# Performance work log

Hardware: AMD Instinct MI355X
Metric: run time of the kernel (lower is better)

## Reference

```python
import jax, jax.numpy as jnp
import numpy as np

B, D, F = 2048, 512, 16384
K = 3
AUX_THR = 0.7
EPS = 1e-8


def setup_inputs() -> dict:
    key = jax.random.key(0)
    ks = jax.random.split(key, 14)
    sc_e = 1.0 / np.sqrt(D)
    sc_d = 1.0 / np.sqrt(F)
    return {
        "model_activations": jax.random.normal(ks[0], (B, D), jnp.float32),
        "We": jax.random.normal(ks[1], (F, D), jnp.float32) * sc_e,
        "be": jax.random.normal(ks[2], (F,), jnp.float32) * 0.01,
        "Wd": jax.random.normal(ks[3], (D, F), jnp.float32) * sc_d,
        "bd": jax.random.normal(ks[4], (D,), jnp.float32) * 0.01,
        "We1": jax.random.normal(ks[5], (F, D), jnp.float32) * sc_e,
        "be1": jax.random.normal(ks[6], (F,), jnp.float32) * 0.01,
        "Wd1": jax.random.normal(ks[7], (D, F), jnp.float32) * sc_d,
        "bd1": jax.random.normal(ks[8], (D,), jnp.float32) * 0.01,
        "We2": jax.random.normal(ks[9], (F, D), jnp.float32) * sc_e,
        "be2": jax.random.normal(ks[10], (F,), jnp.float32) * 0.01,
        "Wd2": jax.random.normal(ks[11], (D, F), jnp.float32) * sc_d,
        "bd2": jax.random.normal(ks[12], (D,), jnp.float32) * 0.01,
    }


def _forward(x, We, be, Wd, bd, We1, be1, Wd1, bd1, We2, be2, Wd2, bd2):
    # parent encoder + top-k scatter
    pre = x @ We.T + be                                   # [B, F]
    vals, idx = jax.lax.top_k(pre, K)                     # [B, K]
    sae = jnp.zeros_like(pre).at[jnp.arange(B)[:, None], idx].set(vals)

    # child routing
    pre1 = x @ We1.T + be1
    pre2 = x @ We2.T + be2
    sae_nz = sae != 0.0
    m1 = jnp.where(sae_nz, pre1, 0.0)
    m2 = jnp.where(sae_nz, pre2, 0.0)
    winners = m1 > m2
    fa1 = jnp.where(winners, m1, 0.0)
    fa2 = jnp.where(~winners, m2, 0.0)

    recon = (sae @ Wd.T + bd) + (fa1 @ Wd1.T + bd1) + (fa2 @ Wd2.T + bd2)

    # live-latent counts (as arrays, jit-friendly)
    n_parent = jnp.zeros((F,), jnp.float32).at[idx.reshape(-1)].set(1.0).sum().astype(jnp.int32)
    n_c1 = jnp.any(fa1 != 0, axis=0).sum().astype(jnp.int32)
    n_c2 = jnp.any(fa2 != 0, axis=0).sum().astype(jnp.int32)

    # auxiliary cosine loss, computed per-feature without materializing
    # the [B, D, F] scaled_parent / combined_weights tensors:
    #   scaled_parent[b,:,f] = a * Wd[:,f],  scaled_child[b,:,f] = c * Wc[:,f]
    # cos over D reduces to per-feature Gram terms.
    pp = jnp.sum(Wd * Wd, axis=0)      # [F] ||Wp_f||^2
    p1 = jnp.sum(Wd * Wd1, axis=0)     # [F] Wp_f . W1_f
    p2 = jnp.sum(Wd * Wd2, axis=0)
    s11 = jnp.sum(Wd1 * Wd1, axis=0)
    s22 = jnp.sum(Wd2 * Wd2, axis=0)

    a = sae                                              # [B, F]
    c = jnp.where(winners, fa1, fa2)                     # [B, F]
    pc = jnp.where(winners, p1[None, :], p2[None, :])    # [B, F]
    cc = jnp.where(winners, s11[None, :], s22[None, :])

    dot = a * (a * pp[None, :] + c * pc)                 # <scaled_parent, combined>
    nx = jnp.abs(a) * jnp.sqrt(pp)[None, :]              # ||scaled_parent||
    ny2 = a * a * pp[None, :] + 2.0 * a * c * pc + c * c * cc
    ny = jnp.sqrt(jnp.maximum(ny2, 0.0))                 # ||combined||
    cos = dot / (jnp.maximum(nx, EPS) * jnp.maximum(ny, EPS))

    active = (a > 0).astype(cos.dtype)
    sim_loss = jnp.maximum(0.0, AUX_THR - cos) * active
    aux = sim_loss.sum() / (active.sum() + 1e-08)

    return recon, (n_parent, n_c1, n_c2), aux


def reference(model_activations, We, be, Wd, bd, We1, be1, Wd1, bd1, We2, be2, Wd2, bd2):
    return _forward(model_activations, We, be, Wd, bd, We1, be1, Wd1, bd1, We2, be2, Wd2, bd2)
```

## Files before the change

kernel.cpp:

```cpp
#include <hip/hip_runtime.h>
#include <math.h>

#define B_DIM 2048
#define D_DIM 512
#define F_DIM 16384
#define K_TOP 3

typedef __attribute__((ext_vector_type(8))) short bf16x8;
typedef __attribute__((ext_vector_type(4))) float f32x4;

#define GL16(gsrc, ldst) \
  __builtin_amdgcn_global_load_lds( \
      (__attribute__((address_space(1))) const void*)(gsrc), \
      (__attribute__((address_space(3))) void*)(ldst), 16, 0, 0)

__device__ __forceinline__ bool better(float v, int c, float w, int j) {
    return (v > w) || (v == w && c < j);
}

__device__ __forceinline__ void ins3(float v, int c,
    float& v0, int& i0, float& v1, int& i1, float& v2, int& i2)
{
    if (!better(v, c, v2, i2)) return;
    if (better(v, c, v1, i1)) {
        v2 = v1; i2 = i1;
        if (better(v, c, v0, i0)) { v1 = v0; i1 = i0; v0 = v; i0 = c; }
        else { v1 = v; i1 = c; }
    } else { v2 = v; i2 = c; }
}

__device__ __forceinline__ uint okey(uint b16, int col) {
    uint m = 0x8000u + ((b16 >> 15) * 0x7FFFu);
    return ((b16 ^ m) << 14) | (uint)(16383 - col);
}

__device__ __forceinline__ void insK8(uint k, uint* V) {
#pragma unroll
    for (int j = 0; j < 8; ++j) {
        uint hi = V[j] > k ? V[j] : k;
        uint lo = V[j] > k ? k : V[j];
        V[j] = hi; k = lo;
    }
}

__device__ __forceinline__ void insK3(uint k, uint& V0, uint& V1, uint& V2) {
    uint h0 = V0 > k ? V0 : k, l0 = V0 > k ? k : V0; V0 = h0; k = l0;
    uint h1 = V1 > k ? V1 : k, l1 = V1 > k ? k : V1; V1 = h1; k = l1;
    V2 = V2 > k ? V2 : k;
}

__device__ __forceinline__ float bf2f(ushort u) {
    return __uint_as_float((uint)u << 16);
}

__global__ __launch_bounds__(256) void convert_kernel(
    const float* __restrict__ We, ushort* __restrict__ We_bf,
    const float* __restrict__ x, ushort* __restrict__ x_bf)
{
    const float* src; ushort* dst; int n8, i, stride;
    if (blockIdx.x < 2048) {
        src = We; dst = We_bf; n8 = F_DIM * D_DIM / 8;
        i = blockIdx.x * 256 + threadIdx.x; stride = 2048 * 256;
    } else {
        src = x; dst = x_bf; n8 = B_DIM * D_DIM / 8;
        i = (blockIdx.x - 2048) * 256 + threadIdx.x; stride = 256 * 256;
    }
    for (; i < n8; i += stride) {
        float4 a = ((const float4*)src)[i * 2];
        float4 b = ((const float4*)src)[i * 2 + 1];
        uint4 o;
        o.x = (__float_as_uint(a.y) & 0xFFFF0000u) | (__float_as_uint(a.x) >> 16);
        o.y = (__float_as_uint(a.w) & 0xFFFF0000u) | (__float_as_uint(a.z) >> 16);
        o.z = (__float_as_uint(b.y) & 0xFFFF0000u) | (__float_as_uint(b.x) >> 16);
        o.w = (__float_as_uint(b.w) & 0xFFFF0000u) | (__float_as_uint(b.z) >> 16);
        ((uint4*)dst)[i] = o;
    }
}

__global__ __launch_bounds__(256) void mega_kernel(
    const ushort* __restrict__ xb, const ushort* __restrict__ web,
    const float* __restrict__ be, uint* __restrict__ packed,
    const float* __restrict__ Wd, const float* __restrict__ Wd1,
    const float* __restrict__ Wd2, ushort* __restrict__ WdT,
    ushort* __restrict__ Wd1T, ushort* __restrict__ Wd2T,
    float* __restrict__ gram)
{
    __shared__ __align__(16) char smem[32768];
    const int t = threadIdx.x;

    if (blockIdx.x < 256) {
        float* tA = (float*)smem;
        float* tB = tA + 32 * 65;
        float* tC = tB + 32 * 65;
        float* gr = tC + 32 * 65;
        const int f0 = blockIdx.x << 6;
        const int fl = t & 63, dgrp = t >> 6;
        const int flw = t >> 2, oct = t & 3;
        float pp = 0, p1 = 0, p2 = 0, s11 = 0, s22 = 0;

        for (int ch = 0; ch < 16; ++ch) {
            const int d0 = ch << 5;
            float a[8], b[8], c[8];
#pragma unroll
            for (int j = 0; j < 8; ++j) {
                int dl = dgrp * 8 + j;
                size_t off = (size_t)(d0 + dl) * F_DIM + f0 + fl;
                a[j] = Wd[off]; b[j] = Wd1[off]; c[j] = Wd2[off];
            }
            if (ch) __syncthreads();
#pragma unroll
            for (int j = 0; j < 8; ++j) {
                pp  = fmaf(a[j], a[j], pp);
                p1  = fmaf(a[j], b[j], p1);
                p2  = fmaf(a[j], c[j], p2);
                s11 = fmaf(b[j], b[j], s11);
                s22 = fmaf(c[j], c[j], s22);
                int dl = dgrp * 8 + j;
                tA[dl * 65 + fl] = a[j];
                tB[dl * 65 + fl] = b[j];
                tC[dl * 65 + fl] = c[j];
            }
            __syncthreads();
            uint4 oa, ob, oc;
            {
                ushort ua[8], ub[8], uc[8];
#pragma unroll
                for (int j = 0; j < 8; ++j) {
                    int dl = oct * 8 + j;
                    ua[j] = (ushort)(__float_as_uint(tA[dl * 65 + flw]) >> 16);
                    ub[j] = (ushort)(__float_as_uint(tB[dl * 65 + flw]) >> 16);
                    uc[j] = (ushort)(__float_as_uint(tC[dl * 65 + flw]) >> 16);
                }
                oa = make_uint4(ua[0] | (ua[1] << 16), ua[2] | (ua[3] << 16),
                                ua[4] | (ua[5] << 16), ua[6] | (ua[7] << 16));
                ob = make_uint4(ub[0] | (ub[1] << 16), ub[2] | (ub[3] << 16),
                                ub[4] | (ub[5] << 16), ub[6] | (ub[7] << 16));
                oc = make_uint4(uc[0] | (uc[1] << 16), uc[2] | (uc[3] << 16),
                                uc[4] | (uc[5] << 16), uc[6] | (uc[7] << 16));
            }
            size_t doff = (size_t)(f0 + flw) * D_DIM + d0 + oct * 8;
            *(uint4*)&WdT[doff]  = oa;
            *(uint4*)&Wd1T[doff] = ob;
            *(uint4*)&Wd2T[doff] = oc;
        }
        __syncthreads();
        gr[(0 * 4 + dgrp) * 64 + fl] = pp;
        gr[(1 * 4 + dgrp) * 64 + fl] = p1;
        gr[(2 * 4 + dgrp) * 64 + fl] = p2;
        gr[(3 * 4 + dgrp) * 64 + fl] = s11;
        gr[(4 * 4 + dgrp) * 64 + fl] = s22;
        __syncthreads();
        if (t < 64) {
#pragma unroll
            for (int s = 0; s < 5; ++s) {
                float g = gr[(s * 4 + 0) * 64 + t] + gr[(s * 4 + 1) * 64 + t]
                        + gr[(s * 4 + 2) * 64 + t] + gr[(s * 4 + 3) * 64 + t];
                gram[s * F_DIM + f0 + t] = g;
            }
        }
        return;
    }

    ushort* As = (ushort*)smem;
    ushort* Bs = As + 8192;
    const int g = blockIdx.x - 256;
    const int l = t & 63;
    const int w = t >> 6;
    const int wr = w >> 1, wc = w & 1;
    const int bm0 = (g >> 7) << 7;
    const int fn0 = (g & 127) << 7;
    const int frow = l & 15;
    const int q = l >> 4;

    const int srow = t >> 2;
    const int sgr = (t & 3) ^ ((t >> 3) & 3);
    const int soff = sgr << 3;
    const ushort* gA0 = xb + (size_t)(bm0 + srow) * D_DIM + soff;
    const ushort* gA1 = xb + (size_t)(bm0 + 64 + srow) * D_DIM + soff;
    const ushort* gB0 = web + (size_t)(fn0 + srow) * D_DIM + soff;
    const ushort* gB1 = web + (size_t)(fn0 + 64 + srow) * D_DIM + soff;

#define STAGE(bufp, koff) do { \
    GL16(gA0 + (koff), (char*)As + (bufp) * 8192 + t * 16); \
    GL16(gA1 + (koff), (char*)As + (bufp) * 8192 + 4096 + t * 16); \
    GL16(gB0 + (koff), (char*)Bs + (bufp) * 8192 + t * 16); \
    GL16(gB1 + (koff), (char*)Bs + (bufp) * 8192 + 4096 + t * 16); \
} while (0)

    f32x4 acc[4][4];
#pragma unroll
    for (int m = 0; m < 4; ++m)
#pragma unroll
        for (int n = 0; n < 4; ++n) acc[m][n] = (f32x4)(0.f);

    STAGE(0, 0);
    __syncthreads();

    const int qs = (q ^ ((frow >> 1) & 3)) << 3;
    const int aoff = (wr * 64 + frow) * 32 + qs;
    const int boff = (wc * 64 + frow) * 32 + qs;

    int cur = 0;
    for (int t16 = 0; t16 < 16; ++t16) {
        const ushort* Ab = As + cur * 4096 + aoff;
        const ushort* Bb = Bs + cur * 4096 + boff;
        bf16x8 af[4], bfr[4];
#pragma unroll
        for (int m = 0; m < 4; ++m) af[m] = *(const bf16x8*)(Ab + m * 512);
#pragma unroll
        for (int n = 0; n < 4; ++n) bfr[n] = *(const bf16x8*)(Bb + n * 512);
        if (t16 < 15) STAGE(cur ^ 1, (t16 + 1) * 32);
#pragma unroll
        for (int m = 0; m < 4; ++m)
#pragma unroll
            for (int n = 0; n < 4; ++n)
                acc[m][n] = __builtin_amdgcn_mfma_f32_16x16x32_bf16(
                    af[m], bfr[n], acc[m][n], 0, 0, 0);
        __syncthreads();
        cur ^= 1;
    }
#undef STAGE

    float bias[4];
#pragma unroll
    for (int n = 0; n < 4; ++n) bias[n] = be[fn0 + wc * 64 + n * 16 + frow];

    const int colb = fn0 + wc * 64 + frow;
    const int rowbase = bm0 + wr * 64 + (q << 2);
    const int tile2 = ((g & 127) << 1) + wc;
#pragma unroll
    for (int m = 0; m < 4; ++m) {
#pragma unroll
        for (int i = 0; i < 4; ++i) {
            uint V0 = 0, V1 = 0, V2 = 0;
#pragma unroll
            for (int n = 0; n < 4; ++n) {
                float v = acc[m][n][i] + bias[n];
                uint key = okey(__float_as_uint(v) >> 16, colb + n * 16);
                insK3(key, V0, V1, V2);
            }
#pragma unroll
            for (int mk = 1; mk <= 8; mk <<= 1) {
                uint o0 = (uint)__shfl_xor((int)V0, mk);
                uint o1 = (uint)__shfl_xor((int)V1, mk);
                uint o2 = (uint)__shfl_xor((int)V2, mk);
                insK3(o0, V0, V1, V2);
                insK3(o1, V0, V1, V2);
                insK3(o2, V0, V1, V2);
            }
            if (frow == 0) {
                uint* dp = packed + (size_t)(rowbase + m * 16 + i) * 768 + tile2 * 3;
                dp[0] = V0; dp[1] = V1; dp[2] = V2;
            }
        }
    }
}

__global__ __launch_bounds__(512) void mergerefine_kernel(
    const uint* __restrict__ packed,
    const float* __restrict__ x, const float* __restrict__ We,
    const float* __restrict__ be,
    float* __restrict__ vals, int* __restrict__ idxv)
{
    __shared__ int sc8[8];
    __shared__ float sv[8];
    __shared__ int si[8];
    const int row = blockIdx.x;
    const int t = threadIdx.x;

    if (t < 64) {
        const uint* p = packed + (size_t)row * 768;
        uint V[8] = {0, 0, 0, 0, 0, 0, 0, 0};
#pragma unroll
        for (int m = 0; m < 12; ++m) {
            uint k = p[t + (m << 6)];
            if (k > V[7]) insK8(k, V);
        }
#pragma unroll
        for (int mk = 1; mk < 64; mk <<= 1) {
            uint o[8];
#pragma unroll
            for (int j = 0; j < 8; ++j) o[j] = (uint)__shfl_xor((int)V[j], mk);
#pragma unroll
            for (int j = 0; j < 8; ++j)
                if (o[j] > V[7]) insK8(o[j], V);
        }
        if (t == 0) {
#pragma unroll
            for (int j = 0; j < 8; ++j)
                sc8[j] = 16383 - (int)(V[j] & 16383u);
        }
    }
    __syncthreads();

    const int wv = t >> 6, l = t & 63;
    const int f = sc8[wv];
    const float* xr = x + (size_t)row * D_DIM;
    const float* wp = We + (size_t)f * D_DIM;
    float s = 0.f;
#pragma unroll
    for (int m = 0; m < 8; ++m) { int e = l + (m << 6); s = fmaf(xr[e], wp[e], s); }
#pragma unroll
    for (int mk = 1; mk < 64; mk <<= 1) s += __shfl_xor(s, mk);
    if (l == 0) { sv[wv] = s + be[f]; si[wv] = f; }
    __syncthreads();
    if (t == 0) {
        float v0 = -INFINITY, v1 = -INFINITY, v2 = -INFINITY;
        int i0 = 0x7fffffff, i1 = 0x7fffffff, i2 = 0x7fffffff;
        for (int k = 0; k < 8; ++k) ins3(sv[k], si[k], v0, i0, v1, i1, v2, i2);
        vals[row * 3 + 0] = v0; idxv[row * 3 + 0] = i0;
        vals[row * 3 + 1] = v1; idxv[row * 3 + 1] = i1;
        vals[row * 3 + 2] = v2; idxv[row * 3 + 2] = i2;
    }
}

__global__ __launch_bounds__(512) void cra_kernel(
    const float* __restrict__ x,
    const float* __restrict__ We1, const float* __restrict__ be1,
    const float* __restrict__ We2, const float* __restrict__ be2,
    const float* __restrict__ vals, const int* __restrict__ idxv,
    const float* __restrict__ gram,
    const ushort* __restrict__ WdT, const float* __restrict__ bd,
    const ushort* __restrict__ Wd1T, const float* __restrict__ bd1,
    const ushort* __restrict__ Wd2T, const float* __restrict__ bd2,
    int* __restrict__ flagP, int* __restrict__ flag1, int* __restrict__ flag2,
    float* __restrict__ auxpart, float* __restrict__ cntpart,
    float* __restrict__ out)
{
    __shared__ float sval[3], sdot[3][2], scv[3], sterm[3], sact[3];
    __shared__ int sidx[3], swin[3];
    const int b = blockIdx.x;
    const int t = threadIdx.x;

    if (t < 3) { sidx[t] = idxv[b * 3 + t]; sval[t] = vals[b * 3 + t]; }
    __syncthreads();

    const int w = t >> 6, l = t & 63;
    if (w < 6) {
        const int p = w >> 1, mt = w & 1;
        const int f = sidx[p];
        const float* wp = (mt ? We2 : We1) + (size_t)f * D_DIM;
        const float* xr = x + (size_t)b * D_DIM;
        float s = 0.f;
#pragma unroll
        for (int m = 0; m < 8; ++m) { int e = l + (m << 6); s = fmaf(xr[e], wp[e], s); }
#pragma unroll
        for (int mk = 1; mk < 64; mk <<= 1) s += __shfl_xor(s, mk);
        if (l == 0) sdot[p][mt] = s + (mt ? be2 : be1)[f];
    }
    __syncthreads();

    if (t < 3) {
        const int p = t;
        const float a = sval[p];
        const int f = sidx[p];
        float m1 = (a != 0.f) ? sdot[p][0] : 0.f;
        float m2 = (a != 0.f) ? sdot[p][1] : 0.f;
        bool win = m1 > m2;
        float fa1 = win ? m1 : 0.f;
        float fa2 = win ? 0.f : m2;
        float cv = win ? fa1 : fa2;
        scv[p] = cv; swin[p] = win ? 1 : 0;
        flagP[f] = 1;
        if (fa1 != 0.f) flag1[f] = 1;
        if (fa2 != 0.f) flag2[f] = 1;
        const float pp = gram[f];
        const float pc = win ? gram[F_DIM + f] : gram[2 * F_DIM + f];
        const float cc = win ? gram[3 * F_DIM + f] : gram[4 * F_DIM + f];
        const float dot = a * (a * pp + cv * pc);
        const float nx = fabsf(a) * sqrtf(pp);
        const float ny2 = a * a * pp + 2.f * a * cv * pc + cv * cv * cc;
        const float ny = sqrtf(fmaxf(ny2, 0.f));
        const float cosv = dot / (fmaxf(nx, 1e-8f) * fmaxf(ny, 1e-8f));
        sterm[p] = (a > 0.f) ? fmaxf(0.f, 0.7f - cosv) : 0.f;
        sact[p] = (a > 0.f) ? 1.f : 0.f;
    }
    __syncthreads();
    if (t == 0) {
        auxpart[b] = sterm[0] + sterm[1] + sterm[2];
        cntpart[b] = sact[0] + sact[1] + sact[2];
    }

    const int d = t;
    float o = bd[d] + bd1[d] + bd2[d];
#pragma unroll
    for (int k = 0; k < 3; ++k) {
        const int f = sidx[k];
        const float a = sval[k];
        const float c = scv[k];
        const int win = swin[k];
        const size_t off = (size_t)f * D_DIM + d;
        o = fmaf(a, bf2f(WdT[off]), o);
        if (c != 0.f) {
            const ushort* wt = win ? Wd1T : Wd2T;
            o = fmaf(c, bf2f(wt[off]), o);
        }
    }
    out[(size_t)b * D_DIM + d] = o;
}

__global__ __launch_bounds__(256) void finalize_kernel(
    const int* __restrict__ flagP, const int* __restrict__ flag1,
    const int* __restrict__ flag2,
    const float* __restrict__ auxpart, const float* __restrict__ cntpart,
    float* __restrict__ out)
{
    const int t = threadIdx.x;
    int sp = 0, s1 = 0, s2 = 0;
    for (int f = t; f < F_DIM; f += 256) { sp += flagP[f]; s1 += flag1[f]; s2 += flag2[f]; }
    float asum = 0.f, acnt = 0.f;
    for (int i = t; i < B_DIM; i += 256) { asum += auxpart[i]; acnt += cntpart[i]; }
#pragma unroll
    for (int m = 1; m < 64; m <<= 1) {
        sp += __shfl_xor(sp, m); s1 += __shfl_xor(s1, m); s2 += __shfl_xor(s2, m);
        asum += __shfl_xor(asum, m); acnt += __shfl_xor(acnt, m);
    }
    __shared__ int red[3][4];
    __shared__ float fred[2][4];
    const int w = t >> 6;
    if ((t & 63) == 0) {
        red[0][w] = sp; red[1][w] = s1; red[2][w] = s2;
        fred[0][w] = asum; fred[1][w] = acnt;
    }
    __syncthreads();
    if (t == 0) {
        float np_ = (float)(red[0][0] + red[0][1] + red[0][2] + red[0][3]);
        float n1_ = (float)(red[1][0] + red[1][1] + red[1][2] + red[1][3]);
        float n2_ = (float)(red[2][0] + red[2][1] + red[2][2] + red[2][3]);
        float as = fred[0][0] + fred[0][1] + fred[0][2] + fred[0][3];
        float ac = fred[1][0] + fred[1][1] + fred[1][2] + fred[1][3];
        const size_t base = (size_t)B_DIM * D_DIM;
        out[base + 0] = np_;
        out[base + 1] = n1_;
        out[base + 2] = n2_;
        out[base + 3] = as / (ac + 1e-8f);
    }
}

extern "C" void kernel_launch(void* const* d_in, const int* in_sizes, int n_in,
                              void* d_out, int out_size, void* d_ws, size_t ws_size,
                              hipStream_t stream)
{
    (void)in_sizes; (void)n_in; (void)out_size; (void)ws_size;
    const float* x   = (const float*)d_in[0];
    const float* We  = (const float*)d_in[1];
    const float* be  = (const float*)d_in[2];
    const float* Wd  = (const float*)d_in[3];
    const float* bd  = (const float*)d_in[4];
    const float* We1 = (const float*)d_in[5];
    const float* be1 = (const float*)d_in[6];
    const float* Wd1 = (const float*)d_in[7];
    const float* bd1 = (const float*)d_in[8];
    const float* We2 = (const float*)d_in[9];
    const float* be2 = (const float*)d_in[10];
    const float* Wd2 = (const float*)d_in[11];
    const float* bd2 = (const float*)d_in[12];
    float* out = (float*)d_out;

    ushort* x_bf  = (ushort*)d_ws;
    ushort* We_bf = x_bf + (size_t)B_DIM * D_DIM;
    ushort* WdT   = We_bf + (size_t)F_DIM * D_DIM;
    ushort* Wd1T  = WdT + (size_t)F_DIM * D_DIM;
    ushort* Wd2T  = Wd1T + (size_t)F_DIM * D_DIM;
    uint*   packed = (uint*)(Wd2T + (size_t)F_DIM * D_DIM);
    float*  gram  = (float*)(packed + (size_t)B_DIM * 768);
    int*    flagP = (int*)(gram + 5 * F_DIM);
    int*    flag1 = flagP + F_DIM;
    int*    flag2 = flag1 + F_DIM;
    float*  vals  = (float*)(flag2 + F_DIM);
    int*    idxv  = (int*)(vals + B_DIM * 3);
    float*  auxpart = (float*)(idxv + B_DIM * 3);
    float*  cntpart = auxpart + B_DIM;

    hipMemsetAsync(flagP, 0, 3 * F_DIM * sizeof(int), stream);

    convert_kernel<<<2304, 256, 0, stream>>>(We, We_bf, x, x_bf);

    mega_kernel<<<2304, 256, 0, stream>>>(
        x_bf, We_bf, be, packed,
        Wd, Wd1, Wd2, WdT, Wd1T, Wd2T, gram);

    mergerefine_kernel<<<B_DIM, 512, 0, stream>>>(
        packed, x, We, be, vals, idxv);

    cra_kernel<<<B_DIM, 512, 0, stream>>>(
        x, We1, be1, We2, be2, vals, idxv, gram,
        WdT, bd, Wd1T, bd1, Wd2T, bd2,
        flagP, flag1, flag2, auxpart, cntpart, out);

    finalize_kernel<<<1, 256, 0, stream>>>(
        flagP, flag1, flag2, auxpart, cntpart, out);
}
```

Before: 152.6 us.

## Split fused mega kernel into separate GEMM and transpose-gram kernels

```diff
diff --git a/kernel.cpp b/kernel.cpp
--- a/kernel.cpp
+++ b/kernel.cpp
@@ -77,98 +77,19 @@
     }
 }
 
-__global__ __launch_bounds__(256) void mega_kernel(
+__global__ __launch_bounds__(256) void gemm_kernel(
     const ushort* __restrict__ xb, const ushort* __restrict__ web,
-    const float* __restrict__ be, uint* __restrict__ packed,
-    const float* __restrict__ Wd, const float* __restrict__ Wd1,
-    const float* __restrict__ Wd2, ushort* __restrict__ WdT,
-    ushort* __restrict__ Wd1T, ushort* __restrict__ Wd2T,
-    float* __restrict__ gram)
-{
-    __shared__ __align__(16) char smem[32768];
+    const float* __restrict__ be, uint* __restrict__ packed)
+{
+    __shared__ __align__(16) ushort As[2][4096];
+    __shared__ __align__(16) ushort Bs[2][4096];
+
     const int t = threadIdx.x;
-
-    if (blockIdx.x < 256) {
-        float* tA = (float*)smem;
-        float* tB = tA + 32 * 65;
-        float* tC = tB + 32 * 65;
-        float* gr = tC + 32 * 65;
-        const int f0 = blockIdx.x << 6;
-        const int fl = t & 63, dgrp = t >> 6;
-        const int flw = t >> 2, oct = t & 3;
-        float pp = 0, p1 = 0, p2 = 0, s11 = 0, s22 = 0;
-
-        for (int ch = 0; ch < 16; ++ch) {
-            const int d0 = ch << 5;
-            float a[8], b[8], c[8];
-#pragma unroll
-            for (int j = 0; j < 8; ++j) {
-                int dl = dgrp * 8 + j;
-                size_t off = (size_t)(d0 + dl) * F_DIM + f0 + fl;
-                a[j] = Wd[off]; b[j] = Wd1[off]; c[j] = Wd2[off];
-            }
-            if (ch) __syncthreads();
-#pragma unroll
-            for (int j = 0; j < 8; ++j) {
-                pp  = fmaf(a[j], a[j], pp);
-                p1  = fmaf(a[j], b[j], p1);
-                p2  = fmaf(a[j], c[j], p2);
-                s11 = fmaf(b[j], b[j], s11);
-                s22 = fmaf(c[j], c[j], s22);
-                int dl = dgrp * 8 + j;
-                tA[dl * 65 + fl] = a[j];
-                tB[dl * 65 + fl] = b[j];
-                tC[dl * 65 + fl] = c[j];
-            }
-            __syncthreads();
-            uint4 oa, ob, oc;
-            {
-                ushort ua[8], ub[8], uc[8];
-#pragma unroll
-                for (int j = 0; j < 8; ++j) {
-                    int dl = oct * 8 + j;
-                    ua[j] = (ushort)(__float_as_uint(tA[dl * 65 + flw]) >> 16);
-                    ub[j] = (ushort)(__float_as_uint(tB[dl * 65 + flw]) >> 16);
-                    uc[j] = (ushort)(__float_as_uint(tC[dl * 65 + flw]) >> 16);
-                }
-                oa = make_uint4(ua[0] | (ua[1] << 16), ua[2] | (ua[3] << 16),
-                                ua[4] | (ua[5] << 16), ua[6] | (ua[7] << 16));
-                ob = make_uint4(ub[0] | (ub[1] << 16), ub[2] | (ub[3] << 16),
-                                ub[4] | (ub[5] << 16), ub[6] | (ub[7] << 16));
-                oc = make_uint4(uc[0] | (uc[1] << 16), uc[2] | (uc[3] << 16),
-                                uc[4] | (uc[5] << 16), uc[6] | (uc[7] << 16));
-            }
-            size_t doff = (size_t)(f0 + flw) * D_DIM + d0 + oct * 8;
-            *(uint4*)&WdT[doff]  = oa;
-            *(uint4*)&Wd1T[doff] = ob;
-            *(uint4*)&Wd2T[doff] = oc;
-        }
-        __syncthreads();
-        gr[(0 * 4 + dgrp) * 64 + fl] = pp;
-        gr[(1 * 4 + dgrp) * 64 + fl] = p1;
-        gr[(2 * 4 + dgrp) * 64 + fl] = p2;
-        gr[(3 * 4 + dgrp) * 64 + fl] = s11;
-        gr[(4 * 4 + dgrp) * 64 + fl] = s22;
-        __syncthreads();
-        if (t < 64) {
-#pragma unroll
-            for (int s = 0; s < 5; ++s) {
-                float g = gr[(s * 4 + 0) * 64 + t] + gr[(s * 4 + 1) * 64 + t]
-                        + gr[(s * 4 + 2) * 64 + t] + gr[(s * 4 + 3) * 64 + t];
-                gram[s * F_DIM + f0 + t] = g;
-            }
-        }
-        return;
-    }
-
-    ushort* As = (ushort*)smem;
-    ushort* Bs = As + 8192;
-    const int g = blockIdx.x - 256;
     const int l = t & 63;
     const int w = t >> 6;
     const int wr = w >> 1, wc = w & 1;
-    const int bm0 = (g >> 7) << 7;
-    const int fn0 = (g & 127) << 7;
+    const int bm0 = blockIdx.y << 7;
+    const int fn0 = blockIdx.x << 7;
     const int frow = l & 15;
     const int q = l >> 4;
 
@@ -202,8 +123,8 @@
 
     int cur = 0;
     for (int t16 = 0; t16 < 16; ++t16) {
-        const ushort* Ab = As + cur * 4096 + aoff;
-        const ushort* Bb = Bs + cur * 4096 + boff;
+        const ushort* Ab = &As[0][0] + cur * 4096 + aoff;
+        const ushort* Bb = &Bs[0][0] + cur * 4096 + boff;
         bf16x8 af[4], bfr[4];
 #pragma unroll
         for (int m = 0; m < 4; ++m) af[m] = *(const bf16x8*)(Ab + m * 512);
@@ -227,7 +148,7 @@
 
     const int colb = fn0 + wc * 64 + frow;
     const int rowbase = bm0 + wr * 64 + (q << 2);
-    const int tile2 = ((g & 127) << 1) + wc;
+    const int tile2 = (blockIdx.x << 1) + wc;
 #pragma unroll
     for (int m = 0; m < 4; ++m) {
 #pragma unroll
@@ -253,6 +174,68 @@
                 dp[0] = V0; dp[1] = V1; dp[2] = V2;
             }
         }
+    }
+}
+
+__global__ __launch_bounds__(512) void trgram_kernel(
+    const float* __restrict__ Wd, const float* __restrict__ Wd1,
+    const float* __restrict__ Wd2, ushort* __restrict__ WdT,
+    ushort* __restrict__ Wd1T, ushort* __restrict__ Wd2T,
+    float* __restrict__ gram)
+{
+    __shared__ float tA[64][65], tB[64][65], tC[64][65];
+    __shared__ float gred[8][64][5];
+    const int t = threadIdx.x;
+    const int f0 = blockIdx.x << 6;
+    const int wg = t >> 6;
+    const int fl = t & 63;
+    float pp = 0, p1 = 0, p2 = 0, s11 = 0, s22 = 0;
+
+    for (int ch = 0; ch < 8; ++ch) {
+        const int d0 = ch << 6;
+        float a[8], b[8], c[8];
+#pragma unroll
+        for (int it = 0; it < 8; ++it) {
+            int dl = (it << 3) + wg;
+            size_t off = (size_t)(d0 + dl) * F_DIM + f0 + fl;
+            a[it] = Wd[off]; b[it] = Wd1[off]; c[it] = Wd2[off];
+        }
+        if (ch) __syncthreads();
+#pragma unroll
+        for (int it = 0; it < 8; ++it) {
+            pp  = fmaf(a[it], a[it], pp);
+            p1  = fmaf(a[it], b[it], p1);
+            p2  = fmaf(a[it], c[it], p2);
+            s11 = fmaf(b[it], b[it], s11);
+            s22 = fmaf(c[it], c[it], s22);
+            int dl = (it << 3) + wg;
+            tA[dl][fl] = a[it]; tB[dl][fl] = b[it]; tC[dl][fl] = c[it];
+        }
+        __syncthreads();
+#pragma unroll
+        for (int it = 0; it < 8; ++it) {
+            int flw = (it << 3) + wg, dlw = fl;
+            size_t doff = (size_t)(f0 + flw) * D_DIM + d0 + dlw;
+            WdT[doff]  = (ushort)(__float_as_uint(tA[dlw][flw]) >> 16);
+            Wd1T[doff] = (ushort)(__float_as_uint(tB[dlw][flw]) >> 16);
+            Wd2T[doff] = (ushort)(__float_as_uint(tC[dlw][flw]) >> 16);
+        }
+    }
+    gred[wg][fl][0] = pp;  gred[wg][fl][1] = p1; gred[wg][fl][2] = p2;
+    gred[wg][fl][3] = s11; gred[wg][fl][4] = s22;
+    __syncthreads();
+    if (t < 64) {
+        float g0 = 0, g1 = 0, g2 = 0, g3 = 0, g4 = 0;
+#pragma unroll
+        for (int g = 0; g < 8; ++g) {
+            g0 += gred[g][t][0]; g1 += gred[g][t][1]; g2 += gred[g][t][2];
+            g3 += gred[g][t][3]; g4 += gred[g][t][4];
+        }
+        gram[f0 + t] = g0;
+        gram[F_DIM + f0 + t] = g1;
+        gram[2 * F_DIM + f0 + t] = g2;
+        gram[3 * F_DIM + f0 + t] = g3;
+        gram[4 * F_DIM + f0 + t] = g4;
     }
 }
 
@@ -476,12 +459,14 @@
 
     convert_kernel<<<2304, 256, 0, stream>>>(We, We_bf, x, x_bf);
 
-    mega_kernel<<<2304, 256, 0, stream>>>(
-        x_bf, We_bf, be, packed,
-        Wd, Wd1, Wd2, WdT, Wd1T, Wd2T, gram);
+    dim3 g1(F_DIM / 128, B_DIM / 128);
+    gemm_kernel<<<g1, 256, 0, stream>>>(x_bf, We_bf, be, packed);
 
     mergerefine_kernel<<<B_DIM, 512, 0, stream>>>(
         packed, x, We, be, vals, idxv);
+
+    trgram_kernel<<<F_DIM / 64, 512, 0, stream>>>(
+        Wd, Wd1, Wd2, WdT, Wd1T, Wd2T, gram);
 
     cra_kernel<<<B_DIM, 512, 0, stream>>>(
         x, We1, be1, We2, be2, vals, idxv, gram,
```

Result: faster. 146.8 us (-3.8%).
